# Performance work log

Hardware: AMD Instinct MI355X
Metric: run time of the kernel (lower is better)

The kernel has to match this reference:

```python
import jax, jax.numpy as jnp
import numpy as np

N, VQ, VK, C, H = 4, 4096, 4096, 128, 64


def setup_inputs() -> dict:
    key = jax.random.key(0)
    kx, ky, kq, kk, kv = jax.random.split(key, 5)
    # xavier-uniform-ish scale for params
    def xavier(k, shape):
        fan_in, fan_out = shape
        lim = (6.0 / (fan_in + fan_out)) ** 0.5
        return jax.random.uniform(k, shape, jnp.float32, -lim, lim)
    return {
        "x": jax.random.normal(kx, (N, VQ, C), jnp.float32),
        "y": jax.random.normal(ky, (N, VK, C), jnp.float32),
        "Wq": xavier(kq, (C, H)),
        "Wk": xavier(kk, (C, H)),
        "Wv": xavier(kv, (C, C)),
    }


def reference(x, y, Wq, Wk, Wv):
    # x: [n, vq, c], y: [n, vk, c]
    scale = Wq.shape[1] ** (-0.5)
    q = jnp.einsum('nvc,co->nvo', x, Wq)   # [n, vq, h]
    k = jnp.einsum('nvc,co->nvo', y, Wk)   # [n, vk, h]
    v = jnp.einsum('nvc,co->nvo', y, Wv)   # [n, vk, c]
    scores = jnp.einsum('nqc,nkc->nqk', q, k) * scale  # [n, vq, vk]
    attn = jax.nn.softmax(scores, axis=-1)
    return jnp.einsum('nqk,nkc->nqc', attn, v)         # [n, vq, c]
```

## Files before the change

kernel.cpp:

```cpp
#include <hip/hip_runtime.h>

typedef __bf16 bf16x8 __attribute__((ext_vector_type(8)));
typedef __bf16 bf16x4 __attribute__((ext_vector_type(4)));
typedef __bf16 bf16x2 __attribute__((ext_vector_type(2)));
typedef float  f32x4  __attribute__((ext_vector_type(4)));
typedef float  f32x16 __attribute__((ext_vector_type(16)));
typedef int    i32x4  __attribute__((ext_vector_type(4)));

#define MFMA16 __builtin_amdgcn_mfma_f32_16x16x32_bf16
#define MFMA32 __builtin_amdgcn_mfma_f32_32x32x16_bf16

static constexpr int BATCH = 4;
static constexpr int SEQ   = 4096;
static constexpr int CDIM  = 128;
static constexpr int HDIM  = 64;
static constexpr float FIXMAX = 16.0f;

union FB2  { bf16x2 h; int i; };
union I4B8 { i32x4 i; bf16x8 b; };

__device__ inline bf16x8 load8f_cvt(const float* __restrict__ p) {
    f32x4 a = *reinterpret_cast<const f32x4*>(p);
    f32x4 b = *reinterpret_cast<const f32x4*>(p + 4);
    bf16x8 r;
    r[0] = (__bf16)a[0]; r[1] = (__bf16)a[1]; r[2] = (__bf16)a[2]; r[3] = (__bf16)a[3];
    r[4] = (__bf16)b[0]; r[5] = (__bf16)b[1]; r[6] = (__bf16)b[2]; r[7] = (__bf16)b[3];
    return r;
}


__global__ __launch_bounds__(256) void proj_all_kernel(
    const float* __restrict__ x, const float* __restrict__ y,
    const float* __restrict__ Wq, const float* __restrict__ Wk,
    const float* __restrict__ Wv,
    __bf16* __restrict__ Qw, __bf16* __restrict__ Kw, __bf16* __restrict__ Vtw,
    float qscale)
{
    __shared__ __bf16 Wt[64][136];
    __shared__ __bf16 Vtile[64][72];

    const int job = blockIdx.x >> 8;
    const int bx  = blockIdx.x & 255;
    const int t    = threadIdx.x;
    const int lane = t & 63;
    const int w    = t >> 6;
    const int m    = lane & 15;
    const int quad = lane >> 4;

    if (job <= 1) {
        const float* X    = job ? y  : x;
        const float* W    = job ? Wk : Wq;
        __bf16*      outp = job ? Kw : Qw;
        const float scale = job ? 1.0f : qscale;

        #pragma unroll
        for (int pass = 0; pass < 4; ++pass) {
            int flat = pass * 2048 + t * 8;
            int cin  = flat >> 6;
            int h0   = flat & 63;
            bf16x8 v = load8f_cvt(W + flat);
            #pragma unroll
            for (int j = 0; j < 8; ++j) Wt[h0 + j][cin] = v[j];
        }
        __syncthreads();

        const int row0 = bx * 64 + w * 16;
        bf16x8 af[4];
        #pragma unroll
        for (int kc = 0; kc < 4; ++kc)
            af[kc] = load8f_cvt(X + (long)(row0 + m) * 128 + kc * 32 + quad * 8);

        #pragma unroll
        for (int tn = 0; tn < 4; ++tn) {
            f32x4 acc = {0.f, 0.f, 0.f, 0.f};
            #pragma unroll
            for (int kc = 0; kc < 4; ++kc) {
                bf16x8 bfrag = *reinterpret_cast<const bf16x8*>(&Wt[tn * 16 + m][kc * 32 + quad * 8]);
                acc = MFMA16(af[kc], bfrag, acc, 0, 0, 0);
            }
            #pragma unroll
            for (int r = 0; r < 4; ++r) {
                int  kg   = row0 + quad * 4 + r;
                long addr = ((long)(kg >> 5) * 4 + tn) * 512
                          + ((m >> 3) * 32 + (kg & 31)) * 8 + (m & 7);
                outp[addr] = (__bf16)(acc[r] * scale);
            }
        }
    } else {
        const int cob = (job - 2) * 64;
        const int ct0 = (job - 2) * 2;

        #pragma unroll
        for (int pass = 0; pass < 4; ++pass) {
            int flat = pass * 2048 + t * 8;
            int cin  = flat >> 6;
            int co0  = flat & 63;
            bf16x8 v = load8f_cvt(Wv + cin * 128 + cob + co0);
            #pragma unroll
            for (int j = 0; j < 8; ++j) Wt[co0 + j][cin] = v[j];
        }
        __syncthreads();

        const int row0 = bx * 64 + w * 16;
        bf16x8 af[4];
        #pragma unroll
        for (int kc = 0; kc < 4; ++kc)
            af[kc] = load8f_cvt(y + (long)(row0 + m) * 128 + kc * 32 + quad * 8);

        #pragma unroll
        for (int tn = 0; tn < 4; ++tn) {
            f32x4 acc = {0.f, 0.f, 0.f, 0.f};
            #pragma unroll
            for (int kc = 0; kc < 4; ++kc) {
                bf16x8 bfrag = *reinterpret_cast<const bf16x8*>(&Wt[tn * 16 + m][kc * 32 + quad * 8]);
                acc = MFMA16(af[kc], bfrag, acc, 0, 0, 0);
            }
            bf16x4 pk;
            #pragma unroll
            for (int r = 0; r < 4; ++r) pk[r] = (__bf16)acc[r];
            *reinterpret_cast<bf16x4*>(&Vtile[tn * 16 + m][w * 16 + quad * 4]) = pk;
        }
        __syncthreads();

        #pragma unroll
        for (int pp = 0; pp < 2; ++pp) {
            int i       = pp * 256 + t;
            int c_local = i & 31;
            int hh      = (i >> 5) & 1;
            int kc2     = (i >> 6) & 1;
            int ct_l    = (i >> 7) & 1;
            int kt_l    = i >> 8;
            bf16x8 v = *reinterpret_cast<const bf16x8*>(
                &Vtile[ct_l * 32 + c_local][kt_l * 32 + kc2 * 16 + hh * 8]);
            long dst = ((long)(bx * 2 + kt_l) * 8 + (ct0 + ct_l) * 2 + kc2) * 512
                     + (hh * 32 + c_local) * 8;
            *reinterpret_cast<bf16x8*>(Vtw + dst) = v;
        }
    }
}

__device__ __forceinline__ void attn_iter(
    const bf16x8 (&qf)[4],
    const bf16x8 (&kf)[4], bf16x8 (&kfn)[4],
    const bf16x8 (&vf)[8], bf16x8 (&vfn)[8],
    const __bf16* __restrict__ kp_next, const __bf16* __restrict__ vp_next,
    bool prefetch, f32x16 (&o_acc)[4], float& l_a, float& l_b, int h)
{
    if (prefetch) {
        #pragma unroll
        for (int kc = 0; kc < 4; ++kc)
            kfn[kc] = *reinterpret_cast<const bf16x8*>(kp_next + kc * 512);
        #pragma unroll
        for (int c = 0; c < 8; ++c)
            vfn[c] = *reinterpret_cast<const bf16x8*>(vp_next + c * 512);
    }

    f32x16 s;
    #pragma unroll
    for (int i = 0; i < 16; ++i) s[i] = -FIXMAX;
    #pragma unroll
    for (int kc = 0; kc < 4; ++kc)
        s = MFMA32(kf[kc], qf[kc], s, 0, 0, 0);

    #pragma unroll
    for (int kc2 = 0; kc2 < 2; ++kc2) {
        int Dw[4];
        #pragma unroll
        for (int r2 = 0; r2 < 4; ++r2) {
            float p0 = __builtin_amdgcn_exp2f(s[8 * kc2 + 2 * r2]);
            float p1 = __builtin_amdgcn_exp2f(s[8 * kc2 + 2 * r2 + 1]);
            l_a += p0; l_b += p1;
            FB2 u; u.h[0] = (__bf16)p0; u.h[1] = (__bf16)p1;
            Dw[r2] = u.i;
        }
        int a0 = Dw[0], a1 = Dw[1], a2 = Dw[2], a3 = Dw[3];
        int r0 = __shfl_xor(a0, 32, 64);
        int r1 = __shfl_xor(a1, 32, 64);
        int r2 = __shfl_xor(a2, 32, 64);
        int r3 = __shfl_xor(a3, 32, 64);
        I4B8 pb;
        pb.i[0] = h ? r2 : a0;
        pb.i[1] = h ? r3 : a1;
        pb.i[2] = h ? a2 : r0;
        pb.i[3] = h ? a3 : r1;
        #pragma unroll
        for (int ct = 0; ct < 4; ++ct)
            o_acc[ct] = MFMA32(vf[ct * 2 + kc2], pb.b, o_acc[ct], 0, 0, 0);
    }
}

__global__ __launch_bounds__(512, 2) void attn_kernel(
    const __bf16* __restrict__ Qs, const __bf16* __restrict__ Ks,
    const __bf16* __restrict__ Vs, float* __restrict__ out)
{
    __shared__ float mbuf[2][2][64][65];

    const int t    = threadIdx.x;
    const int lane = t & 63;
    const int w    = t >> 6;
    const int qs   = w & 1;
    const int g    = w >> 1;
    const int qc   = lane & 31;
    const int h    = lane >> 5;

    const int bxp  = blockIdx.x;
    const int xcd  = bxp & 7;
    const int slot = bxp >> 3;
    const int n    = xcd >> 1;
    const int qtl  = (xcd & 1) * 32 + slot;

    const long QT = (long)n * 128 + qtl * 2 + qs;
    bf16x8 qf[4];
    #pragma unroll
    for (int kc = 0; kc < 4; ++kc)
        qf[kc] = *reinterpret_cast<const bf16x8*>(Qs + (QT * 4 + kc) * 512 + lane * 8);

    const __bf16* kb = Ks + ((long)n * 128 + g * 32) * 2048 + lane * 8;
    const __bf16* vb = Vs + ((long)n * 128 + g * 32) * 4096 + lane * 8;

    f32x16 o_acc[4];
    #pragma unroll
    for (int a = 0; a < 4; ++a)
        #pragma unroll
        for (int i = 0; i < 16; ++i) o_acc[a][i] = 0.f;
    float l_a = 0.f, l_b = 0.f;

    bf16x8 kf0[4], kf1[4];
    bf16x8 vf0[8], vf1[8];

    #pragma unroll
    for (int kc = 0; kc < 4; ++kc)
        kf0[kc] = *reinterpret_cast<const bf16x8*>(kb + kc * 512);
    #pragma unroll
    for (int c = 0; c < 8; ++c)
        vf0[c] = *reinterpret_cast<const bf16x8*>(vb + c * 512);

    for (int kt = 0; kt < 32; kt += 2) {
        attn_iter(qf, kf0, kf1, vf0, vf1,
                  kb + (long)(kt + 1) * 2048, vb + (long)(kt + 1) * 4096,
                  true, o_acc, l_a, l_b, h);
        attn_iter(qf, kf1, kf0, vf1, vf0,
                  kb + (long)(kt + 2) * 2048, vb + (long)(kt + 2) * 4096,
                  kt < 30, o_acc, l_a, l_b, h);
    }

    float l_run = l_a + l_b;

    if (g >= 2) {
        float* dst = &mbuf[qs][g - 2][lane][0];
        #pragma unroll
        for (int ct = 0; ct < 4; ++ct)
            #pragma unroll
            for (int i = 0; i < 16; ++i) dst[ct * 16 + i] = o_acc[ct][i];
        dst[64] = l_run;
    }
    __syncthreads();
    if (g < 2) {
        const float* src = &mbuf[qs][g][lane][0];
        #pragma unroll
        for (int ct = 0; ct < 4; ++ct)
            #pragma unroll
            for (int i = 0; i < 16; ++i) o_acc[ct][i] += src[ct * 16 + i];
        l_run += src[64];
    }
    __syncthreads();
    if (g == 1) {
        float* dst = &mbuf[qs][0][lane][0];
        #pragma unroll
        for (int ct = 0; ct < 4; ++ct)
            #pragma unroll
            for (int i = 0; i < 16; ++i) dst[ct * 16 + i] = o_acc[ct][i];
        dst[64] = l_run;
    }
    __syncthreads();

    if (g == 0) {
        const float* src = &mbuf[qs][0][lane][0];
        #pragma unroll
        for (int ct = 0; ct < 4; ++ct)
            #pragma unroll
            for (int i = 0; i < 16; ++i) o_acc[ct][i] += src[ct * 16 + i];
        l_run += src[64];

        l_run += __shfl_xor(l_run, 32, 64);
        const float inv = 1.0f / l_run;
        const long row = (long)n * SEQ + qtl * 64 + qs * 32 + qc;
        #pragma unroll
        for (int ct = 0; ct < 4; ++ct)
            #pragma unroll
            for (int rg = 0; rg < 4; ++rg) {
                f32x4 o;
                #pragma unroll
                for (int i = 0; i < 4; ++i) o[i] = o_acc[ct][rg * 4 + i] * inv;
                *reinterpret_cast<f32x4*>(
                    out + row * CDIM + ct * 32 + rg * 8 + h * 4) = o;
            }
    }
}

extern "C" void kernel_launch(void* const* d_in, const int* in_sizes, int n_in,
                              void* d_out, int out_size, void* d_ws, size_t ws_size,
                              hipStream_t stream)
{
    const float* x  = (const float*)d_in[0];
    const float* y  = (const float*)d_in[1];
    const float* Wq = (const float*)d_in[2];
    const float* Wk = (const float*)d_in[3];
    const float* Wv = (const float*)d_in[4];
    float* out = (float*)d_out;

    __bf16* Qw  = (__bf16*)d_ws;
    __bf16* Kw  = Qw + (long)BATCH * SEQ * HDIM;
    __bf16* Vtw = Kw + (long)BATCH * SEQ * HDIM;

    const float qscale = 0.125f * 1.4426950408889634f;

    proj_all_kernel<<<dim3(1024), dim3(256), 0, stream>>>(
        x, y, Wq, Wk, Wv, Qw, Kw, Vtw, qscale);

    attn_kernel<<<dim3(256), dim3(512), 0, stream>>>(Qw, Kw, Vtw, out);
}
```

Before: 113.3 us.

## Fuse projection and attention into one kernel with a software grid barrier

Merges the projection kernel and the attention kernel into one launch of 256 blocks. Each block first runs four former projection blocks, two at a time with its two 256-thread halves. It then waits at an atomic grid-wide barrier in workspace before doing attention. Shared memory is unioned between the projection tiles and the reduction buffer. This removes the second launch and the gap between kernels. The cost is a spin-wait barrier that assumes all 256 blocks are resident at once, bounded by a guard counter, plus an extra __syncthreads before the reduction.

```diff
diff --git a/kernel.cpp b/kernel.cpp
--- a/kernel.cpp
+++ b/kernel.cpp
@@ -29,19 +29,26 @@
 }
 
 
-__global__ __launch_bounds__(256) void proj_all_kernel(
+struct ProjSmem {
+    __bf16 Wt[64][136];
+    __bf16 Vtile[64][72];
+};
+
+union FusedSmem {
+    ProjSmem proj[2];
+    float mbuf[2][2][64][65];
+};
+
+__device__ __forceinline__ void proj_block(
+    int oldid, int t, ProjSmem& sp,
     const float* __restrict__ x, const float* __restrict__ y,
     const float* __restrict__ Wq, const float* __restrict__ Wk,
     const float* __restrict__ Wv,
     __bf16* __restrict__ Qw, __bf16* __restrict__ Kw, __bf16* __restrict__ Vtw,
     float qscale)
 {
-    __shared__ __bf16 Wt[64][136];
-    __shared__ __bf16 Vtile[64][72];
-
-    const int job = blockIdx.x >> 8;
-    const int bx  = blockIdx.x & 255;
-    const int t    = threadIdx.x;
+    const int job = oldid >> 8;
+    const int bx  = oldid & 255;
     const int lane = t & 63;
     const int w    = t >> 6;
     const int m    = lane & 15;
@@ -60,7 +67,7 @@
             int h0   = flat & 63;
             bf16x8 v = load8f_cvt(W + flat);
             #pragma unroll
-            for (int j = 0; j < 8; ++j) Wt[h0 + j][cin] = v[j];
+            for (int j = 0; j < 8; ++j) sp.Wt[h0 + j][cin] = v[j];
         }
         __syncthreads();
 
@@ -75,7 +82,7 @@
             f32x4 acc = {0.f, 0.f, 0.f, 0.f};
             #pragma unroll
             for (int kc = 0; kc < 4; ++kc) {
-                bf16x8 bfrag = *reinterpret_cast<const bf16x8*>(&Wt[tn * 16 + m][kc * 32 + quad * 8]);
+                bf16x8 bfrag = *reinterpret_cast<const bf16x8*>(&sp.Wt[tn * 16 + m][kc * 32 + quad * 8]);
                 acc = MFMA16(af[kc], bfrag, acc, 0, 0, 0);
             }
             #pragma unroll
@@ -97,7 +104,7 @@
             int co0  = flat & 63;
             bf16x8 v = load8f_cvt(Wv + cin * 128 + cob + co0);
             #pragma unroll
-            for (int j = 0; j < 8; ++j) Wt[co0 + j][cin] = v[j];
+            for (int j = 0; j < 8; ++j) sp.Wt[co0 + j][cin] = v[j];
         }
         __syncthreads();
 
@@ -112,13 +119,13 @@
             f32x4 acc = {0.f, 0.f, 0.f, 0.f};
             #pragma unroll
             for (int kc = 0; kc < 4; ++kc) {
-                bf16x8 bfrag = *reinterpret_cast<const bf16x8*>(&Wt[tn * 16 + m][kc * 32 + quad * 8]);
+                bf16x8 bfrag = *reinterpret_cast<const bf16x8*>(&sp.Wt[tn * 16 + m][kc * 32 + quad * 8]);
                 acc = MFMA16(af[kc], bfrag, acc, 0, 0, 0);
             }
             bf16x4 pk;
             #pragma unroll
             for (int r = 0; r < 4; ++r) pk[r] = (__bf16)acc[r];
-            *reinterpret_cast<bf16x4*>(&Vtile[tn * 16 + m][w * 16 + quad * 4]) = pk;
+            *reinterpret_cast<bf16x4*>(&sp.Vtile[tn * 16 + m][w * 16 + quad * 4]) = pk;
         }
         __syncthreads();
 
@@ -131,7 +138,7 @@
             int ct_l    = (i >> 7) & 1;
             int kt_l    = i >> 8;
             bf16x8 v = *reinterpret_cast<const bf16x8*>(
-                &Vtile[ct_l * 32 + c_local][kt_l * 32 + kc2 * 16 + hh * 8]);
+                &sp.Vtile[ct_l * 32 + c_local][kt_l * 32 + kc2 * 16 + hh * 8]);
             long dst = ((long)(bx * 2 + kt_l) * 8 + (ct0 + ct_l) * 2 + kc2) * 512
                      + (hh * 32 + c_local) * 8;
             *reinterpret_cast<bf16x8*>(Vtw + dst) = v;
@@ -189,13 +196,56 @@
     }
 }
 
-__global__ __launch_bounds__(512, 2) void attn_kernel(
-    const __bf16* __restrict__ Qs, const __bf16* __restrict__ Ks,
-    const __bf16* __restrict__ Vs, float* __restrict__ out)
+static constexpr unsigned BAR_OPEN = 0x9E3779B9u;
+static constexpr unsigned BAR_DONE = 0x85EBCA77u;
+
+__global__ __launch_bounds__(512, 2) void fused_kernel(
+    const float* __restrict__ x, const float* __restrict__ y,
+    const float* __restrict__ Wq, const float* __restrict__ Wk,
+    const float* __restrict__ Wv,
+    __bf16* __restrict__ Qw, __bf16* __restrict__ Kw, __bf16* __restrict__ Vtw,
+    float* __restrict__ out, float qscale, unsigned* bar)
 {
-    __shared__ float mbuf[2][2][64][65];
+    __shared__ FusedSmem sm;
 
     const int t    = threadIdx.x;
+    const int B    = blockIdx.x;
+    const int half = t >> 8;
+    const int tl   = t & 255;
+
+    if (B == 0 && t == 0) {
+        __hip_atomic_store(bar + 32, 0u, __ATOMIC_RELAXED, __HIP_MEMORY_SCOPE_AGENT);
+        __hip_atomic_store(bar + 0, BAR_OPEN, __ATOMIC_RELEASE, __HIP_MEMORY_SCOPE_AGENT);
+    }
+
+    proj_block(2 * B + half, tl, sm.proj[half], x, y, Wq, Wk, Wv,
+               Qw, Kw, Vtw, qscale);
+    __syncthreads();
+    proj_block(512 + 2 * B + half, tl, sm.proj[half], x, y, Wq, Wk, Wv,
+               Qw, Kw, Vtw, qscale);
+
+    __syncthreads();
+    if (t == 0) {
+        __threadfence();
+        int guard = 0;
+        while (__hip_atomic_load(bar + 0, __ATOMIC_ACQUIRE,
+                                 __HIP_MEMORY_SCOPE_AGENT) != BAR_OPEN
+               && guard < (1 << 24)) { __builtin_amdgcn_s_sleep(8); ++guard; }
+        unsigned my = atomicAdd(bar + 32, 1u) + 1u;
+        if (my == 256u) {
+            __threadfence();
+            __hip_atomic_store(bar + 0, BAR_DONE, __ATOMIC_RELEASE,
+                               __HIP_MEMORY_SCOPE_AGENT);
+        } else {
+            guard = 0;
+            while (__hip_atomic_load(bar + 0, __ATOMIC_ACQUIRE,
+                                     __HIP_MEMORY_SCOPE_AGENT) != BAR_DONE
+                   && guard < (1 << 24)) { __builtin_amdgcn_s_sleep(8); ++guard; }
+        }
+        __threadfence();
+    }
+    __syncthreads();
+
     const int lane = t & 63;
     const int w    = t >> 6;
     const int qs   = w & 1;
@@ -203,9 +253,8 @@
     const int qc   = lane & 31;
     const int h    = lane >> 5;
 
-    const int bxp  = blockIdx.x;
-    const int xcd  = bxp & 7;
-    const int slot = bxp >> 3;
+    const int xcd  = B & 7;
+    const int slot = B >> 3;
     const int n    = xcd >> 1;
     const int qtl  = (xcd & 1) * 32 + slot;
 
@@ -213,10 +262,10 @@
     bf16x8 qf[4];
     #pragma unroll
     for (int kc = 0; kc < 4; ++kc)
-        qf[kc] = *reinterpret_cast<const bf16x8*>(Qs + (QT * 4 + kc) * 512 + lane * 8);
-
-    const __bf16* kb = Ks + ((long)n * 128 + g * 32) * 2048 + lane * 8;
-    const __bf16* vb = Vs + ((long)n * 128 + g * 32) * 4096 + lane * 8;
+        qf[kc] = *reinterpret_cast<const bf16x8*>(Qw + (QT * 4 + kc) * 512 + lane * 8);
+
+    const __bf16* kb = Kw + ((long)n * 128 + g * 32) * 2048 + lane * 8;
+    const __bf16* vb = Vtw + ((long)n * 128 + g * 32) * 4096 + lane * 8;
 
     f32x16 o_acc[4];
     #pragma unroll
@@ -246,8 +295,10 @@
 
     float l_run = l_a + l_b;
 
+    __syncthreads();
+
     if (g >= 2) {
-        float* dst = &mbuf[qs][g - 2][lane][0];
+        float* dst = &sm.mbuf[qs][g - 2][lane][0];
         #pragma unroll
         for (int ct = 0; ct < 4; ++ct)
             #pragma unroll
@@ -256,7 +307,7 @@
     }
     __syncthreads();
     if (g < 2) {
-        const float* src = &mbuf[qs][g][lane][0];
+        const float* src = &sm.mbuf[qs][g][lane][0];
         #pragma unroll
         for (int ct = 0; ct < 4; ++ct)
             #pragma unroll
@@ -265,7 +316,7 @@
     }
     __syncthreads();
     if (g == 1) {
-        float* dst = &mbuf[qs][0][lane][0];
+        float* dst = &sm.mbuf[qs][0][lane][0];
         #pragma unroll
         for (int ct = 0; ct < 4; ++ct)
             #pragma unroll
@@ -275,7 +326,7 @@
     __syncthreads();
 
     if (g == 0) {
-        const float* src = &mbuf[qs][0][lane][0];
+        const float* src = &sm.mbuf[qs][0][lane][0];
         #pragma unroll
         for (int ct = 0; ct < 4; ++ct)
             #pragma unroll
@@ -312,11 +363,10 @@
     __bf16* Qw  = (__bf16*)d_ws;
     __bf16* Kw  = Qw + (long)BATCH * SEQ * HDIM;
     __bf16* Vtw = Kw + (long)BATCH * SEQ * HDIM;
+    unsigned* bar = (unsigned*)((char*)d_ws + (8l << 20));
 
     const float qscale = 0.125f * 1.4426950408889634f;
 
-    proj_all_kernel<<<dim3(1024), dim3(256), 0, stream>>>(
-        x, y, Wq, Wk, Wv, Qw, Kw, Vtw, qscale);
-
-    attn_kernel<<<dim3(256), dim3(512), 0, stream>>>(Qw, Kw, Vtw, out);
-}
+    fused_kernel<<<dim3(256), dim3(512), 0, stream>>>(
+        x, y, Wq, Wk, Wv, Qw, Kw, Vtw, out, qscale, bar);
+}
```

New measurement: 138.3 us. 1.22x slower.

## Stage K/V tiles through LDS with async global_load_lds double buffering

Applied to the files above, without the earlier changes.

Replaces per-wave register prefetch of K and V fragments, where both q-subtile waves loaded the same data, with a shared LDS double buffer. The buffer is filled by global_load_lds direct-to-LDS loads split across the two waves, and barriers plus manual vmcnt waits coordinate it. This halves redundant global/L2 traffic for K/V and frees registers. In exchange it adds LDS reads and two block barriers per tile, and the hand-written vmcnt counts rely on the per-wave load counts being correct.

```diff
diff --git a/kernel.cpp b/kernel.cpp
--- a/kernel.cpp
+++ b/kernel.cpp
@@ -26,6 +26,12 @@
     r[0] = (__bf16)a[0]; r[1] = (__bf16)a[1]; r[2] = (__bf16)a[2]; r[3] = (__bf16)a[3];
     r[4] = (__bf16)b[0]; r[5] = (__bf16)b[1]; r[6] = (__bf16)b[2]; r[7] = (__bf16)b[3];
     return r;
+}
+
+typedef __attribute__((address_space(1))) const unsigned int gas_u32;
+typedef __attribute__((address_space(3))) unsigned int       las_u32;
+__device__ __forceinline__ void stage16(const __bf16* g, __bf16* l) {
+    __builtin_amdgcn_global_load_lds((gas_u32*)g, (las_u32*)l, 16, 0, 0);
 }
 
 
@@ -139,61 +145,14 @@
     }
 }
 
-__device__ __forceinline__ void attn_iter(
-    const bf16x8 (&qf)[4],
-    const bf16x8 (&kf)[4], bf16x8 (&kfn)[4],
-    const bf16x8 (&vf)[8], bf16x8 (&vfn)[8],
-    const __bf16* __restrict__ kp_next, const __bf16* __restrict__ vp_next,
-    bool prefetch, f32x16 (&o_acc)[4], float& l_a, float& l_b, int h)
-{
-    if (prefetch) {
-        #pragma unroll
-        for (int kc = 0; kc < 4; ++kc)
-            kfn[kc] = *reinterpret_cast<const bf16x8*>(kp_next + kc * 512);
-        #pragma unroll
-        for (int c = 0; c < 8; ++c)
-            vfn[c] = *reinterpret_cast<const bf16x8*>(vp_next + c * 512);
-    }
-
-    f32x16 s;
-    #pragma unroll
-    for (int i = 0; i < 16; ++i) s[i] = -FIXMAX;
-    #pragma unroll
-    for (int kc = 0; kc < 4; ++kc)
-        s = MFMA32(kf[kc], qf[kc], s, 0, 0, 0);
-
-    #pragma unroll
-    for (int kc2 = 0; kc2 < 2; ++kc2) {
-        int Dw[4];
-        #pragma unroll
-        for (int r2 = 0; r2 < 4; ++r2) {
-            float p0 = __builtin_amdgcn_exp2f(s[8 * kc2 + 2 * r2]);
-            float p1 = __builtin_amdgcn_exp2f(s[8 * kc2 + 2 * r2 + 1]);
-            l_a += p0; l_b += p1;
-            FB2 u; u.h[0] = (__bf16)p0; u.h[1] = (__bf16)p1;
-            Dw[r2] = u.i;
-        }
-        int a0 = Dw[0], a1 = Dw[1], a2 = Dw[2], a3 = Dw[3];
-        int r0 = __shfl_xor(a0, 32, 64);
-        int r1 = __shfl_xor(a1, 32, 64);
-        int r2 = __shfl_xor(a2, 32, 64);
-        int r3 = __shfl_xor(a3, 32, 64);
-        I4B8 pb;
-        pb.i[0] = h ? r2 : a0;
-        pb.i[1] = h ? r3 : a1;
-        pb.i[2] = h ? a2 : r0;
-        pb.i[3] = h ? a3 : r1;
-        #pragma unroll
-        for (int ct = 0; ct < 4; ++ct)
-            o_acc[ct] = MFMA32(vf[ct * 2 + kc2], pb.b, o_acc[ct], 0, 0, 0);
-    }
-}
-
 __global__ __launch_bounds__(512, 2) void attn_kernel(
     const __bf16* __restrict__ Qs, const __bf16* __restrict__ Ks,
     const __bf16* __restrict__ Vs, float* __restrict__ out)
 {
-    __shared__ float mbuf[2][2][64][65];
+    __shared__ union {
+        struct { __bf16 K[2][4][4][512]; __bf16 V[2][4][8][512]; } st;
+        float mbuf[2][2][64][65];
+    } sm;
 
     const int t    = threadIdx.x;
     const int lane = t & 63;
@@ -218,6 +177,22 @@
     const __bf16* kb = Ks + ((long)n * 128 + g * 32) * 2048 + lane * 8;
     const __bf16* vb = Vs + ((long)n * 128 + g * 32) * 4096 + lane * 8;
 
+    auto stage_tile = [&](int tt) {
+        const int b = tt & 1;
+        if (qs == 0) {
+            #pragma unroll
+            for (int kc = 0; kc < 4; ++kc)
+                stage16(kb + ((long)tt * 4 + kc) * 512, &sm.st.K[b][g][kc][0]);
+            #pragma unroll
+            for (int c = 0; c < 2; ++c)
+                stage16(vb + ((long)tt * 8 + c) * 512, &sm.st.V[b][g][c][0]);
+        } else {
+            #pragma unroll
+            for (int c = 2; c < 8; ++c)
+                stage16(vb + ((long)tt * 8 + c) * 512, &sm.st.V[b][g][c][0]);
+        }
+    };
+
     f32x16 o_acc[4];
     #pragma unroll
     for (int a = 0; a < 4; ++a)
@@ -225,29 +200,62 @@
         for (int i = 0; i < 16; ++i) o_acc[a][i] = 0.f;
     float l_a = 0.f, l_b = 0.f;
 
-    bf16x8 kf0[4], kf1[4];
-    bf16x8 vf0[8], vf1[8];
-
-    #pragma unroll
-    for (int kc = 0; kc < 4; ++kc)
-        kf0[kc] = *reinterpret_cast<const bf16x8*>(kb + kc * 512);
-    #pragma unroll
-    for (int c = 0; c < 8; ++c)
-        vf0[c] = *reinterpret_cast<const bf16x8*>(vb + c * 512);
-
-    for (int kt = 0; kt < 32; kt += 2) {
-        attn_iter(qf, kf0, kf1, vf0, vf1,
-                  kb + (long)(kt + 1) * 2048, vb + (long)(kt + 1) * 4096,
-                  true, o_acc, l_a, l_b, h);
-        attn_iter(qf, kf1, kf0, vf1, vf0,
-                  kb + (long)(kt + 2) * 2048, vb + (long)(kt + 2) * 4096,
-                  kt < 30, o_acc, l_a, l_b, h);
+    stage_tile(0);
+    stage_tile(1);
+
+    for (int kt = 0; kt < 32; ++kt) {
+        if (kt < 31) asm volatile("s_waitcnt vmcnt(6)" ::: "memory");
+        else         asm volatile("s_waitcnt vmcnt(0)" ::: "memory");
+        __builtin_amdgcn_s_barrier();
+
+        const int p = kt & 1;
+
+        f32x16 s;
+        #pragma unroll
+        for (int i = 0; i < 16; ++i) s[i] = -FIXMAX;
+        #pragma unroll
+        for (int kc = 0; kc < 4; ++kc) {
+            bf16x8 kf = *reinterpret_cast<const bf16x8*>(&sm.st.K[p][g][kc][lane * 8]);
+            s = MFMA32(kf, qf[kc], s, 0, 0, 0);
+        }
+
+        #pragma unroll
+        for (int kc2 = 0; kc2 < 2; ++kc2) {
+            int Dw[4];
+            #pragma unroll
+            for (int r2 = 0; r2 < 4; ++r2) {
+                float p0 = __builtin_amdgcn_exp2f(s[8 * kc2 + 2 * r2]);
+                float p1 = __builtin_amdgcn_exp2f(s[8 * kc2 + 2 * r2 + 1]);
+                l_a += p0; l_b += p1;
+                FB2 u; u.h[0] = (__bf16)p0; u.h[1] = (__bf16)p1;
+                Dw[r2] = u.i;
+            }
+            int a0 = Dw[0], a1 = Dw[1], a2 = Dw[2], a3 = Dw[3];
+            int r0 = __shfl_xor(a0, 32, 64);
+            int r1 = __shfl_xor(a1, 32, 64);
+            int r2 = __shfl_xor(a2, 32, 64);
+            int r3 = __shfl_xor(a3, 32, 64);
+            I4B8 pb;
+            pb.i[0] = h ? r2 : a0;
+            pb.i[1] = h ? r3 : a1;
+            pb.i[2] = h ? a2 : r0;
+            pb.i[3] = h ? a3 : r1;
+            #pragma unroll
+            for (int ct = 0; ct < 4; ++ct) {
+                bf16x8 vf = *reinterpret_cast<const bf16x8*>(
+                    &sm.st.V[p][g][ct * 2 + kc2][lane * 8]);
+                o_acc[ct] = MFMA32(vf, pb.b, o_acc[ct], 0, 0, 0);
+            }
+        }
+
+        __builtin_amdgcn_s_barrier();
+        if (kt < 30) stage_tile(kt + 2);
     }
 
     float l_run = l_a + l_b;
 
     if (g >= 2) {
-        float* dst = &mbuf[qs][g - 2][lane][0];
+        float* dst = &sm.mbuf[qs][g - 2][lane][0];
         #pragma unroll
         for (int ct = 0; ct < 4; ++ct)
             #pragma unroll
@@ -256,7 +264,7 @@
     }
     __syncthreads();
     if (g < 2) {
-        const float* src = &mbuf[qs][g][lane][0];
+        const float* src = &sm.mbuf[qs][g][lane][0];
         #pragma unroll
         for (int ct = 0; ct < 4; ++ct)
             #pragma unroll
@@ -265,7 +273,7 @@
     }
     __syncthreads();
     if (g == 1) {
-        float* dst = &mbuf[qs][0][lane][0];
+        float* dst = &sm.mbuf[qs][0][lane][0];
         #pragma unroll
         for (int ct = 0; ct < 4; ++ct)
             #pragma unroll
@@ -275,7 +283,7 @@
     __syncthreads();
 
     if (g == 0) {
-        const float* src = &mbuf[qs][0][lane][0];
+        const float* src = &sm.mbuf[qs][0][lane][0];
         #pragma unroll
         for (int ct = 0; ct < 4; ++ct)
             #pragma unroll
```

New measurement: 146.4 us. 29.3% more time.
